# Kernel tuning notes

Measured on AMD Instinct MI355X. Metric: run time of the kernel, lower is better.

## Reference

```python
import jax, jax.numpy as jnp
import numpy as np

N_POINTS = 50000   # rows of features, also number of output segments
N_EDGES = 1600000  # ragged neighborhood edges (out_idx, in_idx)
CHANNELS = 64


def setup_inputs() -> dict:
    key = jax.random.key(0)
    k1, k2 = jax.random.split(key)
    features = jax.random.normal(k1, (N_POINTS, CHANNELS), dtype=jnp.float32)
    sparse_indices = jax.random.randint(
        k2, (N_EDGES, 2), 0, N_POINTS, dtype=jnp.int64
    )
    return {"features": features, "sparse_indices": sparse_indices}


def reference(features, sparse_indices):
    # sparse_indices[:, 0] = output segment id, sparse_indices[:, 1] = input row.
    out_idx = sparse_indices[:, 0]
    in_idx = sparse_indices[:, 1]
    gathered = features[in_idx]  # [E, C] gather of neighbor features
    # Unsorted segment max over the ragged neighborhoods -> [N, C].
    pooled = jax.ops.segment_max(gathered, out_idx, num_segments=N_POINTS)
    return pooled
```

## Files before the change

### kernel.cpp

```cpp
#include <hip/hip_runtime.h>
#include <hip/hip_bf16.h>
#include <math.h>


#define N_POINTS 50000
#define N_EDGES  1600000
#define CHANNELS 64
#define BIN_SHIFT 6
#define BIN_PTS   64
#define NBINS     782
#define NBINS_PAD 1024
#define CAPL      2560
#define QCAP      2560
#define P1_GRID   256
#define P1_BLK    1024
#define ECHUNK    (N_EDGES / P1_GRID)
#define ECHUNK_PAD 6256
#define CVT_TOTAL (N_POINTS * CHANNELS / 4)
#define CVT_PER   ((CVT_TOTAL + P1_GRID - 1) / P1_GRID)

__device__ __forceinline__ unsigned int encode_bf16(float x) {
    unsigned int u = __float_as_uint(x);
    unsigned int r = ((u >> 16) & 1u) + 0x7FFFu;
    unsigned int h = (u + r) >> 16;
    return (h & 0x8000u) ? (h ^ 0xFFFFu) : (h | 0x8000u);
}

__device__ __forceinline__ float decode_u16(unsigned int v) {
    if (v == 0u) return -INFINITY;
    unsigned int h = (v & 0x8000u) ? (v ^ 0x8000u) : (v ^ 0xFFFFu);
    return __uint_as_float(h << 16);
}

__device__ __forceinline__ unsigned int pk_max_u16(unsigned int a, unsigned int b) {
    unsigned int d;
    asm("v_pk_max_u16 %0, %1, %2" : "=v"(d) : "v"(a), "v"(b));
    return d;
}

__global__ __launch_bounds__(P1_BLK) void binsort_cvt_kernel(
    const int2*   __restrict__ idx,
    const float4* __restrict__ feat4,
    uint2*        __restrict__ f16o,
    unsigned int* __restrict__ chunkd,
    unsigned int* __restrict__ pfxg)
{
    __shared__ unsigned int hist[NBINS_PAD];
    __shared__ unsigned int pfx[NBINS_PAD];
    __shared__ __align__(16) unsigned int staging[ECHUNK_PAD];
    __shared__ unsigned int wsum[16];

    int tid  = threadIdx.x;
    int lane = tid & 63, w = tid >> 6;

    {
        int cb = blockIdx.x * CVT_PER;
        #pragma unroll
        for (int k = 0; k < 4; ++k) {
            int i = cb + k * P1_BLK + tid;
            if (i < cb + CVT_PER && i < CVT_TOTAL) {
                float4 v = feat4[i];
                uint2 r;
                r.x = encode_bf16(v.x) | (encode_bf16(v.y) << 16);
                r.y = encode_bf16(v.z) | (encode_bf16(v.w) << 16);
                f16o[i] = r;
            }
        }
    }

    int base = blockIdx.x * ECHUNK;

    hist[tid] = 0u;
    __syncthreads();

    int2 e[7]; unsigned int slot[7];
    #pragma unroll
    for (int j = 0; j < 7; ++j) {
        int i = j * P1_BLK + tid;
        if (i < ECHUNK) {
            e[j] = idx[base + i];
            slot[j] = atomicAdd(&hist[(unsigned)e[j].x >> BIN_SHIFT], 1u);
        }
    }
    __syncthreads();

    {
        unsigned int a = hist[tid];
        unsigned int inc = a;
        #pragma unroll
        for (int d = 1; d < 64; d <<= 1) {
            unsigned int v = __shfl_up(inc, d, 64);
            if (lane >= d) inc += v;
        }
        if (lane == 63) wsum[w] = inc;
        __syncthreads();
        unsigned int woff = 0;
        #pragma unroll
        for (int k = 0; k < 16; ++k) if (k < w) woff += wsum[k];
        pfx[tid] = woff + inc - a;
    }
    __syncthreads();

    #pragma unroll
    for (int j = 0; j < 7; ++j) {
        int i = j * P1_BLK + tid;
        if (i < ECHUNK) {
            unsigned int dst = (unsigned)e[j].x, src = (unsigned)e[j].y;
            unsigned int bin = dst >> BIN_SHIFT;
            staging[pfx[bin] + slot[j]] =
                (bin << 22) | ((dst & (BIN_PTS - 1)) << 16) | src;
        }
    }
    if (tid < ECHUNK_PAD - ECHUNK) staging[ECHUNK + tid] = 0u;
    __syncthreads();

    {
        const uint4* st4 = (const uint4*)staging;
        uint4* cd4 = (uint4*)(chunkd + (size_t)blockIdx.x * ECHUNK_PAD);
        #pragma unroll
        for (int k = 0; k < 2; ++k) {
            int i = k * P1_BLK + tid;
            if (i < ECHUNK_PAD / 4) cd4[i] = st4[i];
        }
        pfxg[blockIdx.x * NBINS_PAD + tid] = pfx[tid];
    }
}

__global__ __launch_bounds__(512) void pool_kernel(
    const unsigned int* __restrict__ feat16,
    const unsigned int* __restrict__ chunkd,
    const unsigned int* __restrict__ pfxg,
    float4* __restrict__ out4)
{
    __shared__ unsigned int list[CAPL];
    __shared__ unsigned int sorted[QCAP];
    __shared__ unsigned int choff[P1_GRID];
    __shared__ unsigned int hist[64];
    __shared__ unsigned int start[65];
    __shared__ unsigned int cur[64];
    __shared__ unsigned int wsum4[4];
    __shared__ unsigned int Tsh;

    int tid = threadIdx.x;
    int bin = blockIdx.x;
    int lane = tid & 63, w = tid >> 6;

    if (tid < 64) hist[tid] = 0u;

    unsigned int cntc = 0, segs = 0, inc = 0;
    if (tid < P1_GRID) {
        unsigned int s = pfxg[tid * NBINS_PAD + bin];
        unsigned int e = pfxg[tid * NBINS_PAD + bin + 1];
        segs = s; cntc = e - s;
        inc = cntc;
        #pragma unroll
        for (int d = 1; d < 64; d <<= 1) {
            unsigned int v = __shfl_up(inc, d, 64);
            if (lane >= d) inc += v;
        }
        if (lane == 63) wsum4[w] = inc;
    }
    __syncthreads();
    if (tid < P1_GRID) {
        unsigned int woff = 0;
        #pragma unroll
        for (int k = 0; k < 4; ++k) if (k < w) woff += wsum4[k];
        unsigned int off = woff + inc - cntc;
        choff[tid] = off;
        if (tid == P1_GRID - 1) Tsh = off + cntc;
    }
    __syncthreads();

    unsigned int T = Tsh; if (T > CAPL) T = CAPL;

    {
        int c = tid >> 1, h = tid & 1;
        unsigned int s = pfxg[c * NBINS_PAD + bin];
        unsigned int e = pfxg[c * NBINS_PAD + bin + 1];
        unsigned int n = e - s;
        unsigned int off = choff[c];
        unsigned int g0 = (unsigned)c * ECHUNK_PAD + s;
        for (unsigned int j = h; j < n; j += 2) {
            unsigned int v = chunkd[g0 + j];
            if (off + j < CAPL) list[off + j] = v;
        }
    }
    __syncthreads();

    for (unsigned int t = tid; t < T; t += 512)
        atomicAdd(&hist[(list[t] >> 16) & 63], 1u);
    __syncthreads();

    if (tid < 64) {
        unsigned int h = hist[tid], inc2 = h;
        #pragma unroll
        for (int d = 1; d < 64; d <<= 1) {
            unsigned int v = __shfl_up(inc2, d, 64);
            if (tid >= d) inc2 += v;
        }
        start[tid] = inc2 - h; cur[tid] = inc2 - h;
        if (tid == 63) start[64] = inc2;
    }
    __syncthreads();

    for (unsigned int t = tid; t < T; t += 512) {
        unsigned int v = list[t];
        unsigned int slot = atomicAdd(&cur[(v >> 16) & 63], 1u);
        if (slot < QCAP) sorted[slot] = (v & 0xFFFFu) << 3;
    }
    __syncthreads();

    const uint4* frow = (const uint4*)feat16;
    int g = tid >> 3, ln = tid & 7;
    unsigned int s0 = start[g], s1 = start[g + 1];
    if (s1 > QCAP) s1 = QCAP;

    unsigned int A0=0,A1=0,A2=0,A3=0, B0=0,B1=0,B2=0,B3=0;
    unsigned int C0=0,C1=0,C2=0,C3=0, D0=0,D1=0,D2=0,D3=0;
    unsigned int i = s0;
    for (; i + 4 <= s1; i += 4) {
        unsigned int r0 = sorted[i+0], r1 = sorted[i+1];
        unsigned int r2 = sorted[i+2], r3 = sorted[i+3];
        uint4 u0 = frow[r0 + ln];
        uint4 u1 = frow[r1 + ln];
        uint4 u2 = frow[r2 + ln];
        uint4 u3 = frow[r3 + ln];
        A0 = pk_max_u16(A0, u0.x); A1 = pk_max_u16(A1, u0.y);
        A2 = pk_max_u16(A2, u0.z); A3 = pk_max_u16(A3, u0.w);
        B0 = pk_max_u16(B0, u1.x); B1 = pk_max_u16(B1, u1.y);
        B2 = pk_max_u16(B2, u1.z); B3 = pk_max_u16(B3, u1.w);
        C0 = pk_max_u16(C0, u2.x); C1 = pk_max_u16(C1, u2.y);
        C2 = pk_max_u16(C2, u2.z); C3 = pk_max_u16(C3, u2.w);
        D0 = pk_max_u16(D0, u3.x); D1 = pk_max_u16(D1, u3.y);
        D2 = pk_max_u16(D2, u3.z); D3 = pk_max_u16(D3, u3.w);
    }
    for (; i < s1; ++i) {
        uint4 u = frow[sorted[i] + ln];
        A0 = pk_max_u16(A0, u.x); A1 = pk_max_u16(A1, u.y);
        A2 = pk_max_u16(A2, u.z); A3 = pk_max_u16(A3, u.w);
    }
    A0 = pk_max_u16(pk_max_u16(A0, B0), pk_max_u16(C0, D0));
    A1 = pk_max_u16(pk_max_u16(A1, B1), pk_max_u16(C1, D1));
    A2 = pk_max_u16(pk_max_u16(A2, B2), pk_max_u16(C2, D2));
    A3 = pk_max_u16(pk_max_u16(A3, B3), pk_max_u16(C3, D3));

    int gp = bin * BIN_PTS + g;
    if (gp < N_POINTS) {
        float4 o0, o1;
        o0.x = decode_u16(A0 & 0xFFFFu); o0.y = decode_u16(A0 >> 16);
        o0.z = decode_u16(A1 & 0xFFFFu); o0.w = decode_u16(A1 >> 16);
        o1.x = decode_u16(A2 & 0xFFFFu); o1.y = decode_u16(A2 >> 16);
        o1.z = decode_u16(A3 & 0xFFFFu); o1.w = decode_u16(A3 >> 16);
        out4[(size_t)gp * 16 + ln * 2 + 0] = o0;
        out4[(size_t)gp * 16 + ln * 2 + 1] = o1;
    }
}

extern "C" void kernel_launch(void* const* d_in, const int* in_sizes, int n_in,
                              void* d_out, int out_size, void* d_ws, size_t ws_size,
                              hipStream_t stream) {
    const float4* feat4 = (const float4*)d_in[0];
    const int2*   idx   = (const int2*)d_in[1];

    size_t off_feat16 = 0;
    size_t off_chunk  = (size_t)N_POINTS * CHANNELS * 2;
    size_t off_pfxg   = off_chunk + (size_t)P1_GRID * ECHUNK_PAD * 4;
    uint2*        f16o   = (uint2*)((char*)d_ws + off_feat16);
    unsigned int* feat16 = (unsigned int*)((char*)d_ws + off_feat16);
    unsigned int* chunkd = (unsigned int*)((char*)d_ws + off_chunk);
    unsigned int* pfxg   = (unsigned int*)((char*)d_ws + off_pfxg);

    binsort_cvt_kernel<<<P1_GRID, P1_BLK, 0, stream>>>(idx, feat4, f16o, chunkd, pfxg);
    pool_kernel<<<NBINS, 512, 0, stream>>>(feat16, chunkd, pfxg, (float4*)d_out);
}
```

Before: 104.6 us.

## Halve bin size to 32 points and split each segment's edges across two lane groups

```diff
diff --git a/kernel.cpp b/kernel.cpp
--- a/kernel.cpp
+++ b/kernel.cpp
@@ -6,12 +6,11 @@
 #define N_POINTS 50000
 #define N_EDGES  1600000
 #define CHANNELS 64
-#define BIN_SHIFT 6
-#define BIN_PTS   64
-#define NBINS     782
-#define NBINS_PAD 1024
-#define CAPL      2560
-#define QCAP      2560
+#define BIN_SHIFT 5
+#define BIN_PTS   32
+#define NBINS     1563
+#define NBINS_PAD 2048
+#define CAPL      1536
 #define P1_GRID   256
 #define P1_BLK    1024
 #define ECHUNK    (N_EDGES / P1_GRID)
@@ -71,6 +70,7 @@
     int base = blockIdx.x * ECHUNK;
 
     hist[tid] = 0u;
+    hist[tid + P1_BLK] = 0u;
     __syncthreads();
 
     int2 e[7]; unsigned int slot[7];
@@ -85,8 +85,8 @@
     __syncthreads();
 
     {
-        unsigned int a = hist[tid];
-        unsigned int inc = a;
+        unsigned int h0 = hist[2 * tid], h1 = hist[2 * tid + 1];
+        unsigned int s = h0 + h1, inc = s;
         #pragma unroll
         for (int d = 1; d < 64; d <<= 1) {
             unsigned int v = __shfl_up(inc, d, 64);
@@ -97,7 +97,9 @@
         unsigned int woff = 0;
         #pragma unroll
         for (int k = 0; k < 16; ++k) if (k < w) woff += wsum[k];
-        pfx[tid] = woff + inc - a;
+        unsigned int b = woff + inc - s;
+        pfx[2 * tid]     = b;
+        pfx[2 * tid + 1] = b + h0;
     }
     __syncthreads();
 
@@ -108,7 +110,7 @@
             unsigned int dst = (unsigned)e[j].x, src = (unsigned)e[j].y;
             unsigned int bin = dst >> BIN_SHIFT;
             staging[pfx[bin] + slot[j]] =
-                (bin << 22) | ((dst & (BIN_PTS - 1)) << 16) | src;
+                (bin << 21) | ((dst & (BIN_PTS - 1)) << 16) | src;
         }
     }
     if (tid < ECHUNK_PAD - ECHUNK) staging[ECHUNK + tid] = 0u;
@@ -122,7 +124,8 @@
             int i = k * P1_BLK + tid;
             if (i < ECHUNK_PAD / 4) cd4[i] = st4[i];
         }
-        pfxg[blockIdx.x * NBINS_PAD + tid] = pfx[tid];
+        pfxg[(size_t)blockIdx.x * NBINS_PAD + tid] = pfx[tid];
+        pfxg[(size_t)blockIdx.x * NBINS_PAD + tid + P1_BLK] = pfx[tid + P1_BLK];
     }
 }
 
@@ -133,11 +136,11 @@
     float4* __restrict__ out4)
 {
     __shared__ unsigned int list[CAPL];
-    __shared__ unsigned int sorted[QCAP];
+    __shared__ unsigned int sorted[CAPL];
     __shared__ unsigned int choff[P1_GRID];
-    __shared__ unsigned int hist[64];
-    __shared__ unsigned int start[65];
-    __shared__ unsigned int cur[64];
+    __shared__ unsigned int hist[32];
+    __shared__ unsigned int start[33];
+    __shared__ unsigned int cur[32];
     __shared__ unsigned int wsum4[4];
     __shared__ unsigned int Tsh;
 
@@ -145,13 +148,13 @@
     int bin = blockIdx.x;
     int lane = tid & 63, w = tid >> 6;
 
-    if (tid < 64) hist[tid] = 0u;
-
-    unsigned int cntc = 0, segs = 0, inc = 0;
+    if (tid < 32) hist[tid] = 0u;
+
+    unsigned int cntc = 0, inc = 0;
     if (tid < P1_GRID) {
-        unsigned int s = pfxg[tid * NBINS_PAD + bin];
-        unsigned int e = pfxg[tid * NBINS_PAD + bin + 1];
-        segs = s; cntc = e - s;
+        unsigned int s = pfxg[(size_t)tid * NBINS_PAD + bin];
+        unsigned int e = pfxg[(size_t)tid * NBINS_PAD + bin + 1];
+        cntc = e - s;
         inc = cntc;
         #pragma unroll
         for (int d = 1; d < 64; d <<= 1) {
@@ -175,8 +178,8 @@
 
     {
         int c = tid >> 1, h = tid & 1;
-        unsigned int s = pfxg[c * NBINS_PAD + bin];
-        unsigned int e = pfxg[c * NBINS_PAD + bin + 1];
+        unsigned int s = pfxg[(size_t)c * NBINS_PAD + bin];
+        unsigned int e = pfxg[(size_t)c * NBINS_PAD + bin + 1];
         unsigned int n = e - s;
         unsigned int off = choff[c];
         unsigned int g0 = (unsigned)c * ECHUNK_PAD + s;
@@ -188,39 +191,39 @@
     __syncthreads();
 
     for (unsigned int t = tid; t < T; t += 512)
-        atomicAdd(&hist[(list[t] >> 16) & 63], 1u);
-    __syncthreads();
-
-    if (tid < 64) {
+        atomicAdd(&hist[(list[t] >> 16) & 31], 1u);
+    __syncthreads();
+
+    if (tid < 32) {
         unsigned int h = hist[tid], inc2 = h;
         #pragma unroll
-        for (int d = 1; d < 64; d <<= 1) {
-            unsigned int v = __shfl_up(inc2, d, 64);
+        for (int d = 1; d < 32; d <<= 1) {
+            unsigned int v = __shfl_up(inc2, d, 32);
             if (tid >= d) inc2 += v;
         }
         start[tid] = inc2 - h; cur[tid] = inc2 - h;
-        if (tid == 63) start[64] = inc2;
+        if (tid == 31) start[32] = inc2;
     }
     __syncthreads();
 
     for (unsigned int t = tid; t < T; t += 512) {
         unsigned int v = list[t];
-        unsigned int slot = atomicAdd(&cur[(v >> 16) & 63], 1u);
-        if (slot < QCAP) sorted[slot] = (v & 0xFFFFu) << 3;
+        unsigned int slot = atomicAdd(&cur[(v >> 16) & 31], 1u);
+        if (slot < CAPL) sorted[slot] = (v & 0xFFFFu) << 3;
     }
     __syncthreads();
 
     const uint4* frow = (const uint4*)feat16;
-    int g = tid >> 3, ln = tid & 7;
+    int g = tid >> 4, l16 = tid & 15, sg = l16 >> 3, ln = l16 & 7;
     unsigned int s0 = start[g], s1 = start[g + 1];
-    if (s1 > QCAP) s1 = QCAP;
+    if (s1 > CAPL) s1 = CAPL;
 
     unsigned int A0=0,A1=0,A2=0,A3=0, B0=0,B1=0,B2=0,B3=0;
     unsigned int C0=0,C1=0,C2=0,C3=0, D0=0,D1=0,D2=0,D3=0;
-    unsigned int i = s0;
-    for (; i + 4 <= s1; i += 4) {
-        unsigned int r0 = sorted[i+0], r1 = sorted[i+1];
-        unsigned int r2 = sorted[i+2], r3 = sorted[i+3];
+    unsigned int i = s0 + sg;
+    for (; i + 6 < s1; i += 8) {
+        unsigned int r0 = sorted[i+0], r1 = sorted[i+2];
+        unsigned int r2 = sorted[i+4], r3 = sorted[i+6];
         uint4 u0 = frow[r0 + ln];
         uint4 u1 = frow[r1 + ln];
         uint4 u2 = frow[r2 + ln];
@@ -234,7 +237,7 @@
         D0 = pk_max_u16(D0, u3.x); D1 = pk_max_u16(D1, u3.y);
         D2 = pk_max_u16(D2, u3.z); D3 = pk_max_u16(D3, u3.w);
     }
-    for (; i < s1; ++i) {
+    for (; i < s1; i += 2) {
         uint4 u = frow[sorted[i] + ln];
         A0 = pk_max_u16(A0, u.x); A1 = pk_max_u16(A1, u.y);
         A2 = pk_max_u16(A2, u.z); A3 = pk_max_u16(A3, u.w);
@@ -244,8 +247,13 @@
     A2 = pk_max_u16(pk_max_u16(A2, B2), pk_max_u16(C2, D2));
     A3 = pk_max_u16(pk_max_u16(A3, B3), pk_max_u16(C3, D3));
 
+    A0 = pk_max_u16(A0, (unsigned int)__shfl_xor((int)A0, 8));
+    A1 = pk_max_u16(A1, (unsigned int)__shfl_xor((int)A1, 8));
+    A2 = pk_max_u16(A2, (unsigned int)__shfl_xor((int)A2, 8));
+    A3 = pk_max_u16(A3, (unsigned int)__shfl_xor((int)A3, 8));
+
     int gp = bin * BIN_PTS + g;
-    if (gp < N_POINTS) {
+    if (gp < N_POINTS && sg == 0) {
         float4 o0, o1;
         o0.x = decode_u16(A0 & 0xFFFFu); o0.y = decode_u16(A0 >> 16);
         o0.z = decode_u16(A1 & 0xFFFFu); o0.w = decode_u16(A1 >> 16);
```

After: 108.6 us. 3.8% more time.

## Split pool kernel channels across two blocks per bin

Applied to the files above, without the earlier changes.

```diff
diff --git a/kernel.cpp b/kernel.cpp
--- a/kernel.cpp
+++ b/kernel.cpp
@@ -18,6 +18,7 @@
 #define ECHUNK_PAD 6256
 #define CVT_TOTAL (N_POINTS * CHANNELS / 4)
 #define CVT_PER   ((CVT_TOTAL + P1_GRID - 1) / P1_GRID)
+#define P2_GRID   1568
 
 __device__ __forceinline__ unsigned int encode_bf16(float x) {
     unsigned int u = __float_as_uint(x);
@@ -142,16 +143,20 @@
     __shared__ unsigned int Tsh;
 
     int tid = threadIdx.x;
-    int bin = blockIdx.x;
+    int bid = blockIdx.x;
+    int half = (bid >> 2) & 1;
+    int bin  = (bid >> 3) * 4 + (bid & 3);
+    if (bin >= NBINS) return;
+
     int lane = tid & 63, w = tid >> 6;
 
     if (tid < 64) hist[tid] = 0u;
 
-    unsigned int cntc = 0, segs = 0, inc = 0;
+    unsigned int cntc = 0, inc = 0;
     if (tid < P1_GRID) {
         unsigned int s = pfxg[tid * NBINS_PAD + bin];
         unsigned int e = pfxg[tid * NBINS_PAD + bin + 1];
-        segs = s; cntc = e - s;
+        cntc = e - s;
         inc = cntc;
         #pragma unroll
         for (int d = 1; d < 64; d <<= 1) {
@@ -206,53 +211,43 @@
     for (unsigned int t = tid; t < T; t += 512) {
         unsigned int v = list[t];
         unsigned int slot = atomicAdd(&cur[(v >> 16) & 63], 1u);
-        if (slot < QCAP) sorted[slot] = (v & 0xFFFFu) << 3;
-    }
-    __syncthreads();
-
-    const uint4* frow = (const uint4*)feat16;
+        if (slot < QCAP) sorted[slot] = (v & 0xFFFFu) << 4;
+    }
+    __syncthreads();
+
+    const uint2* frow2 = (const uint2*)feat16;
     int g = tid >> 3, ln = tid & 7;
+    unsigned int hoff = (unsigned)half * 8 + (unsigned)ln;
     unsigned int s0 = start[g], s1 = start[g + 1];
     if (s1 > QCAP) s1 = QCAP;
 
-    unsigned int A0=0,A1=0,A2=0,A3=0, B0=0,B1=0,B2=0,B3=0;
-    unsigned int C0=0,C1=0,C2=0,C3=0, D0=0,D1=0,D2=0,D3=0;
+    unsigned int A0=0,A1=0, B0=0,B1=0, C0=0,C1=0, D0=0,D1=0;
     unsigned int i = s0;
     for (; i + 4 <= s1; i += 4) {
         unsigned int r0 = sorted[i+0], r1 = sorted[i+1];
         unsigned int r2 = sorted[i+2], r3 = sorted[i+3];
-        uint4 u0 = frow[r0 + ln];
-        uint4 u1 = frow[r1 + ln];
-        uint4 u2 = frow[r2 + ln];
-        uint4 u3 = frow[r3 + ln];
+        uint2 u0 = frow2[r0 + hoff];
+        uint2 u1 = frow2[r1 + hoff];
+        uint2 u2 = frow2[r2 + hoff];
+        uint2 u3 = frow2[r3 + hoff];
         A0 = pk_max_u16(A0, u0.x); A1 = pk_max_u16(A1, u0.y);
-        A2 = pk_max_u16(A2, u0.z); A3 = pk_max_u16(A3, u0.w);
         B0 = pk_max_u16(B0, u1.x); B1 = pk_max_u16(B1, u1.y);
-        B2 = pk_max_u16(B2, u1.z); B3 = pk_max_u16(B3, u1.w);
         C0 = pk_max_u16(C0, u2.x); C1 = pk_max_u16(C1, u2.y);
-        C2 = pk_max_u16(C2, u2.z); C3 = pk_max_u16(C3, u2.w);
         D0 = pk_max_u16(D0, u3.x); D1 = pk_max_u16(D1, u3.y);
-        D2 = pk_max_u16(D2, u3.z); D3 = pk_max_u16(D3, u3.w);
     }
     for (; i < s1; ++i) {
-        uint4 u = frow[sorted[i] + ln];
+        uint2 u = frow2[sorted[i] + hoff];
         A0 = pk_max_u16(A0, u.x); A1 = pk_max_u16(A1, u.y);
-        A2 = pk_max_u16(A2, u.z); A3 = pk_max_u16(A3, u.w);
     }
     A0 = pk_max_u16(pk_max_u16(A0, B0), pk_max_u16(C0, D0));
     A1 = pk_max_u16(pk_max_u16(A1, B1), pk_max_u16(C1, D1));
-    A2 = pk_max_u16(pk_max_u16(A2, B2), pk_max_u16(C2, D2));
-    A3 = pk_max_u16(pk_max_u16(A3, B3), pk_max_u16(C3, D3));
 
     int gp = bin * BIN_PTS + g;
     if (gp < N_POINTS) {
-        float4 o0, o1;
-        o0.x = decode_u16(A0 & 0xFFFFu); o0.y = decode_u16(A0 >> 16);
-        o0.z = decode_u16(A1 & 0xFFFFu); o0.w = decode_u16(A1 >> 16);
-        o1.x = decode_u16(A2 & 0xFFFFu); o1.y = decode_u16(A2 >> 16);
-        o1.z = decode_u16(A3 & 0xFFFFu); o1.w = decode_u16(A3 >> 16);
-        out4[(size_t)gp * 16 + ln * 2 + 0] = o0;
-        out4[(size_t)gp * 16 + ln * 2 + 1] = o1;
+        float4 o;
+        o.x = decode_u16(A0 & 0xFFFFu); o.y = decode_u16(A0 >> 16);
+        o.z = decode_u16(A1 & 0xFFFFu); o.w = decode_u16(A1 >> 16);
+        out4[(size_t)gp * 16 + hoff] = o;
     }
 }
 
@@ -271,5 +266,5 @@
     unsigned int* pfxg   = (unsigned int*)((char*)d_ws + off_pfxg);
 
     binsort_cvt_kernel<<<P1_GRID, P1_BLK, 0, stream>>>(idx, feat4, f16o, chunkd, pfxg);
-    pool_kernel<<<NBINS, 512, 0, stream>>>(feat16, chunkd, pfxg, (float4*)d_out);
-}
+    pool_kernel<<<P2_GRID, 512, 0, stream>>>(feat16, chunkd, pfxg, (float4*)d_out);
+}
```

Measured after the change: 124.4 us. 1.19x slower.

## Split bf16 feature table into channel halves and gather each in separate pass

Applied to the files above, without the earlier changes.

```diff
diff --git a/kernel.cpp b/kernel.cpp
--- a/kernel.cpp
+++ b/kernel.cpp
@@ -41,7 +41,8 @@
 __global__ __launch_bounds__(P1_BLK) void binsort_cvt_kernel(
     const int2*   __restrict__ idx,
     const float4* __restrict__ feat4,
-    uint2*        __restrict__ f16o,
+    uint2*        __restrict__ f16a,
+    uint2*        __restrict__ f16b,
     unsigned int* __restrict__ chunkd,
     unsigned int* __restrict__ pfxg)
 {
@@ -63,7 +64,9 @@
                 uint2 r;
                 r.x = encode_bf16(v.x) | (encode_bf16(v.y) << 16);
                 r.y = encode_bf16(v.z) | (encode_bf16(v.w) << 16);
-                f16o[i] = r;
+                int p = i >> 4, q = i & 15;
+                if (q < 8) f16a[p * 8 + q] = r;
+                else       f16b[p * 8 + (q - 8)] = r;
             }
         }
     }
@@ -126,10 +129,69 @@
     }
 }
 
-__global__ __launch_bounds__(512) void pool_kernel(
-    const unsigned int* __restrict__ feat16,
+__device__ __forceinline__ void gather_half(
+    const uint4* __restrict__ fh4,
+    const unsigned int* __restrict__ sorted,
+    const unsigned int* __restrict__ start,
+    float4* __restrict__ out4, int bin, int half, int tid)
+{
+    int g = tid >> 3, ln = tid & 7;
+    int el = ln >> 2, l4 = ln & 3;
+    unsigned int s0 = start[g], s1 = start[g + 1];
+    if (s1 > QCAP) s1 = QCAP;
+
+    unsigned int A0=0,A1=0,A2=0,A3=0, B0=0,B1=0,B2=0,B3=0;
+    unsigned int C0=0,C1=0,C2=0,C3=0, D0=0,D1=0,D2=0,D3=0;
+    unsigned int i = s0 + (unsigned)el;
+    for (; i + 6 < s1; i += 8) {
+        unsigned int r0 = sorted[i+0], r1 = sorted[i+2];
+        unsigned int r2 = sorted[i+4], r3 = sorted[i+6];
+        uint4 u0 = fh4[r0 + l4];
+        uint4 u1 = fh4[r1 + l4];
+        uint4 u2 = fh4[r2 + l4];
+        uint4 u3 = fh4[r3 + l4];
+        A0 = pk_max_u16(A0, u0.x); A1 = pk_max_u16(A1, u0.y);
+        A2 = pk_max_u16(A2, u0.z); A3 = pk_max_u16(A3, u0.w);
+        B0 = pk_max_u16(B0, u1.x); B1 = pk_max_u16(B1, u1.y);
+        B2 = pk_max_u16(B2, u1.z); B3 = pk_max_u16(B3, u1.w);
+        C0 = pk_max_u16(C0, u2.x); C1 = pk_max_u16(C1, u2.y);
+        C2 = pk_max_u16(C2, u2.z); C3 = pk_max_u16(C3, u2.w);
+        D0 = pk_max_u16(D0, u3.x); D1 = pk_max_u16(D1, u3.y);
+        D2 = pk_max_u16(D2, u3.z); D3 = pk_max_u16(D3, u3.w);
+    }
+    for (; i < s1; i += 2) {
+        uint4 u = fh4[sorted[i] + l4];
+        A0 = pk_max_u16(A0, u.x); A1 = pk_max_u16(A1, u.y);
+        A2 = pk_max_u16(A2, u.z); A3 = pk_max_u16(A3, u.w);
+    }
+    A0 = pk_max_u16(pk_max_u16(A0, B0), pk_max_u16(C0, D0));
+    A1 = pk_max_u16(pk_max_u16(A1, B1), pk_max_u16(C1, D1));
+    A2 = pk_max_u16(pk_max_u16(A2, B2), pk_max_u16(C2, D2));
+    A3 = pk_max_u16(pk_max_u16(A3, B3), pk_max_u16(C3, D3));
+
+    A0 = pk_max_u16(A0, (unsigned int)__shfl_xor((int)A0, 4));
+    A1 = pk_max_u16(A1, (unsigned int)__shfl_xor((int)A1, 4));
+    A2 = pk_max_u16(A2, (unsigned int)__shfl_xor((int)A2, 4));
+    A3 = pk_max_u16(A3, (unsigned int)__shfl_xor((int)A3, 4));
+
+    int gp = bin * BIN_PTS + g;
+    if (gp < N_POINTS && el == 0) {
+        float4 o0, o1;
+        o0.x = decode_u16(A0 & 0xFFFFu); o0.y = decode_u16(A0 >> 16);
+        o0.z = decode_u16(A1 & 0xFFFFu); o0.w = decode_u16(A1 >> 16);
+        o1.x = decode_u16(A2 & 0xFFFFu); o1.y = decode_u16(A2 >> 16);
+        o1.z = decode_u16(A3 & 0xFFFFu); o1.w = decode_u16(A3 >> 16);
+        out4[(size_t)gp * 16 + half * 8 + l4 * 2 + 0] = o0;
+        out4[(size_t)gp * 16 + half * 8 + l4 * 2 + 1] = o1;
+    }
+}
+
+__global__ __launch_bounds__(512) void pool_a_kernel(
+    const unsigned int* __restrict__ f16a,
     const unsigned int* __restrict__ chunkd,
     const unsigned int* __restrict__ pfxg,
+    unsigned int* __restrict__ sortedg,
+    unsigned int* __restrict__ startg,
     float4* __restrict__ out4)
 {
     __shared__ unsigned int list[CAPL];
@@ -147,11 +209,11 @@
 
     if (tid < 64) hist[tid] = 0u;
 
-    unsigned int cntc = 0, segs = 0, inc = 0;
+    unsigned int cntc = 0, inc = 0;
     if (tid < P1_GRID) {
         unsigned int s = pfxg[tid * NBINS_PAD + bin];
         unsigned int e = pfxg[tid * NBINS_PAD + bin + 1];
-        segs = s; cntc = e - s;
+        cntc = e - s;
         inc = cntc;
         #pragma unroll
         for (int d = 1; d < 64; d <<= 1) {
@@ -206,54 +268,37 @@
     for (unsigned int t = tid; t < T; t += 512) {
         unsigned int v = list[t];
         unsigned int slot = atomicAdd(&cur[(v >> 16) & 63], 1u);
-        if (slot < QCAP) sorted[slot] = (v & 0xFFFFu) << 3;
-    }
-    __syncthreads();
-
-    const uint4* frow = (const uint4*)feat16;
-    int g = tid >> 3, ln = tid & 7;
-    unsigned int s0 = start[g], s1 = start[g + 1];
-    if (s1 > QCAP) s1 = QCAP;
-
-    unsigned int A0=0,A1=0,A2=0,A3=0, B0=0,B1=0,B2=0,B3=0;
-    unsigned int C0=0,C1=0,C2=0,C3=0, D0=0,D1=0,D2=0,D3=0;
-    unsigned int i = s0;
-    for (; i + 4 <= s1; i += 4) {
-        unsigned int r0 = sorted[i+0], r1 = sorted[i+1];
-        unsigned int r2 = sorted[i+2], r3 = sorted[i+3];
-        uint4 u0 = frow[r0 + ln];
-        uint4 u1 = frow[r1 + ln];
-        uint4 u2 = frow[r2 + ln];
-        uint4 u3 = frow[r3 + ln];
-        A0 = pk_max_u16(A0, u0.x); A1 = pk_max_u16(A1, u0.y);
-        A2 = pk_max_u16(A2, u0.z); A3 = pk_max_u16(A3, u0.w);
-        B0 = pk_max_u16(B0, u1.x); B1 = pk_max_u16(B1, u1.y);
-        B2 = pk_max_u16(B2, u1.z); B3 = pk_max_u16(B3, u1.w);
-        C0 = pk_max_u16(C0, u2.x); C1 = pk_max_u16(C1, u2.y);
-        C2 = pk_max_u16(C2, u2.z); C3 = pk_max_u16(C3, u2.w);
-        D0 = pk_max_u16(D0, u3.x); D1 = pk_max_u16(D1, u3.y);
-        D2 = pk_max_u16(D2, u3.z); D3 = pk_max_u16(D3, u3.w);
-    }
-    for (; i < s1; ++i) {
-        uint4 u = frow[sorted[i] + ln];
-        A0 = pk_max_u16(A0, u.x); A1 = pk_max_u16(A1, u.y);
-        A2 = pk_max_u16(A2, u.z); A3 = pk_max_u16(A3, u.w);
-    }
-    A0 = pk_max_u16(pk_max_u16(A0, B0), pk_max_u16(C0, D0));
-    A1 = pk_max_u16(pk_max_u16(A1, B1), pk_max_u16(C1, D1));
-    A2 = pk_max_u16(pk_max_u16(A2, B2), pk_max_u16(C2, D2));
-    A3 = pk_max_u16(pk_max_u16(A3, B3), pk_max_u16(C3, D3));
-
-    int gp = bin * BIN_PTS + g;
-    if (gp < N_POINTS) {
-        float4 o0, o1;
-        o0.x = decode_u16(A0 & 0xFFFFu); o0.y = decode_u16(A0 >> 16);
-        o0.z = decode_u16(A1 & 0xFFFFu); o0.w = decode_u16(A1 >> 16);
-        o1.x = decode_u16(A2 & 0xFFFFu); o1.y = decode_u16(A2 >> 16);
-        o1.z = decode_u16(A3 & 0xFFFFu); o1.w = decode_u16(A3 >> 16);
-        out4[(size_t)gp * 16 + ln * 2 + 0] = o0;
-        out4[(size_t)gp * 16 + ln * 2 + 1] = o1;
-    }
+        if (slot < QCAP) sorted[slot] = (v & 0xFFFFu) << 2;
+    }
+    __syncthreads();
+
+    for (unsigned int t = tid; t < T; t += 512)
+        sortedg[(size_t)bin * QCAP + t] = sorted[t];
+    if (tid < 65) startg[bin * 65 + tid] = start[tid];
+
+    gather_half((const uint4*)f16a, sorted, start, out4, bin, 0, tid);
+}
+
+__global__ __launch_bounds__(512) void pool_b_kernel(
+    const unsigned int* __restrict__ f16b,
+    const unsigned int* __restrict__ sortedg,
+    const unsigned int* __restrict__ startg,
+    float4* __restrict__ out4)
+{
+    __shared__ unsigned int sorted[QCAP];
+    __shared__ unsigned int start[65];
+
+    int tid = threadIdx.x;
+    int bin = blockIdx.x;
+
+    if (tid < 65) start[tid] = startg[bin * 65 + tid];
+    __syncthreads();
+    unsigned int T = start[64]; if (T > QCAP) T = QCAP;
+    for (unsigned int t = tid; t < T; t += 512)
+        sorted[t] = sortedg[(size_t)bin * QCAP + t];
+    __syncthreads();
+
+    gather_half((const uint4*)f16b, sorted, start, out4, bin, 1, tid);
 }
 
 extern "C" void kernel_launch(void* const* d_in, const int* in_sizes, int n_in,
@@ -262,14 +307,23 @@
     const float4* feat4 = (const float4*)d_in[0];
     const int2*   idx   = (const int2*)d_in[1];
 
-    size_t off_feat16 = 0;
-    size_t off_chunk  = (size_t)N_POINTS * CHANNELS * 2;
+    size_t off_f16a   = 0;
+    size_t off_f16b   = (size_t)N_POINTS * CHANNELS;
+    size_t off_chunk  = off_f16b + (size_t)N_POINTS * CHANNELS;
     size_t off_pfxg   = off_chunk + (size_t)P1_GRID * ECHUNK_PAD * 4;
-    uint2*        f16o   = (uint2*)((char*)d_ws + off_feat16);
-    unsigned int* feat16 = (unsigned int*)((char*)d_ws + off_feat16);
-    unsigned int* chunkd = (unsigned int*)((char*)d_ws + off_chunk);
-    unsigned int* pfxg   = (unsigned int*)((char*)d_ws + off_pfxg);
-
-    binsort_cvt_kernel<<<P1_GRID, P1_BLK, 0, stream>>>(idx, feat4, f16o, chunkd, pfxg);
-    pool_kernel<<<NBINS, 512, 0, stream>>>(feat16, chunkd, pfxg, (float4*)d_out);
-}
+    size_t off_sorted = off_pfxg + (size_t)P1_GRID * NBINS_PAD * 4;
+    size_t off_startg = off_sorted + (size_t)NBINS * QCAP * 4;
+    uint2*        f16a    = (uint2*)((char*)d_ws + off_f16a);
+    uint2*        f16b    = (uint2*)((char*)d_ws + off_f16b);
+    unsigned int* chunkd  = (unsigned int*)((char*)d_ws + off_chunk);
+    unsigned int* pfxg    = (unsigned int*)((char*)d_ws + off_pfxg);
+    unsigned int* sortedg = (unsigned int*)((char*)d_ws + off_sorted);
+    unsigned int* startg  = (unsigned int*)((char*)d_ws + off_startg);
+
+    binsort_cvt_kernel<<<P1_GRID, P1_BLK, 0, stream>>>(idx, feat4, f16a, f16b,
+                                                       chunkd, pfxg);
+    pool_a_kernel<<<NBINS, 512, 0, stream>>>((const unsigned int*)f16a, chunkd,
+                                             pfxg, sortedg, startg, (float4*)d_out);
+    pool_b_kernel<<<NBINS, 512, 0, stream>>>((const unsigned int*)f16b, sortedg,
+                                             startg, (float4*)d_out);
+}
```

After: 114.5 us. 9.4% more time.
